# Performance work log

Hardware: AMD Instinct MI355X
Metric: run time of the kernel (lower is better)

Reference implementation:

```python
import jax, jax.numpy as jnp
import numpy as np

N, E, F, EB, NB, G = 50000, 800000, 64, 20, 3, 100
CUTOFF = 5.0
NUM_EMB = 119


def silu(x):
    return x * jax.nn.sigmoid(x)


def setup_inputs() -> dict:
    key = jax.random.key(0)
    ks = jax.random.split(key, 16)
    w = lambda k, shape, scale: jax.random.normal(k, shape, dtype=jnp.float32) * scale
    inp = {}
    # forward args
    inp["node_features"] = jax.random.randint(ks[0], (N,), 1, NUM_EMB)
    inp["node_positions"] = jax.random.normal(ks[1], (N, 3), dtype=jnp.float32)
    inp["edge_index"] = jax.random.randint(ks[2], (2, E), 0, N)
    inp["node_graph_index"] = jnp.sort(jax.random.randint(ks[3], (N,), 0, G))
    # learned parameters (stacked over NB interaction blocks)
    inp["emb"] = w(ks[4], (NUM_EMB, F), 1.0)
    inp["msg_W1"] = w(ks[5], (NB, F, F), F ** -0.5)
    inp["msg_b1"] = jnp.zeros((NB, F), jnp.float32)
    inp["msg_W2"] = w(ks[6], (NB, F, 3 * F), F ** -0.5)
    inp["msg_b2"] = jnp.zeros((NB, 3 * F), jnp.float32)
    inp["filt_W"] = w(ks[7], (NB, EB, 3 * F), EB ** -0.5)
    inp["filt_b"] = jnp.zeros((NB, 3 * F), jnp.float32)
    inp["upd_U"] = w(ks[8], (NB, F, F), F ** -0.5)
    inp["upd_V"] = w(ks[9], (NB, F, F), F ** -0.5)
    inp["upd_W1"] = w(ks[10], (NB, 2 * F, F), (2 * F) ** -0.5)
    inp["upd_b1"] = jnp.zeros((NB, F), jnp.float32)
    inp["upd_W2"] = w(ks[11], (NB, F, 3 * F), F ** -0.5)
    inp["upd_b2"] = jnp.zeros((NB, 3 * F), jnp.float32)
    # readout MLP: Linear(F,F) + SiLU + Linear(F,1)
    inp["ro_W1"] = w(ks[12], (F, F), F ** -0.5)
    inp["ro_b1"] = jnp.zeros((F,), jnp.float32)
    inp["ro_W2"] = w(ks[13], (F, 1), F ** -0.5)
    inp["ro_b2"] = jnp.zeros((1,), jnp.float32)
    return inp


def _painn_forward(node_positions, emb, msg_W1, msg_b1, msg_W2, msg_b2,
                   filt_W, filt_b, upd_U, upd_V, upd_W1, upd_b1, upd_W2, upd_b2,
                   ro_W1, ro_b1, ro_W2, ro_b2,
                   node_features, edge_index, node_graph_index):
    recv, send = edge_index[0], edge_index[1]  # row aggregates over col neighbors
    s = emb[node_features]                      # [N,F] scalar node states
    v = jnp.zeros((N, 3, F), s.dtype)           # [N,3,F] vector node states

    # edge geometry
    d = node_positions[send] - node_positions[recv]       # [E,3]
    r = jnp.sqrt(jnp.sum(d * d, axis=1, keepdims=True))   # [E,1]
    dhat = d / (r + 1e-10)                                # unit edge vectors

    # Bessel (sinc) radial basis expansion of edge norms: [E,EB]
    n = jnp.arange(1, EB + 1, dtype=s.dtype)
    rbf = jnp.sqrt(2.0 / CUTOFF) * jnp.sin(n * jnp.pi * r / CUTOFF) / (r + 1e-10)
    # smooth cosine cutoff: [E,1]
    fc = jnp.where(r < CUTOFF, 0.5 * (jnp.cos(jnp.pi * r / CUTOFF) + 1.0), 0.0)

    for b in range(NB):
        # --- message block ---
        phi = silu(s @ msg_W1[b] + msg_b1[b]) @ msg_W2[b] + msg_b2[b]   # [N,3F]
        Wf = (rbf @ filt_W[b] + filt_b[b]) * fc                          # [E,3F]
        m = phi[send] * Wf                                               # [E,3F]
        gate_v, gate_e, m_s = jnp.split(m, 3, axis=-1)                   # [E,F] each
        m_v = v[send] * gate_v[:, None, :] + dhat[:, :, None] * gate_e[:, None, :]  # [E,3,F]
        s = s + jax.ops.segment_sum(m_s, recv, num_segments=N)
        v = v + jax.ops.segment_sum(m_v, recv, num_segments=N)
        # --- update block ---
        Uv = jnp.einsum('ndf,fg->ndg', v, upd_U[b])                      # [N,3,F]
        Vv = jnp.einsum('ndf,fg->ndg', v, upd_V[b])                      # [N,3,F]
        Vn = jnp.sqrt(jnp.sum(Vv * Vv, axis=1) + 1e-8)                   # [N,F]
        a = silu(jnp.concatenate([s, Vn], axis=-1) @ upd_W1[b] + upd_b1[b]) @ upd_W2[b] + upd_b2[b]
        a_vv, a_sv, a_ss = jnp.split(a, 3, axis=-1)
        v = v + a_vv[:, None, :] * Uv
        s = s + a_sv * jnp.sum(Uv * Vv, axis=1) + a_ss

    # readout MLP + per-graph sum reduction
    ro = silu(s @ ro_W1 + ro_b1) @ ro_W2 + ro_b2                         # [N,1]
    graph_out = jax.ops.segment_sum(ro, node_graph_index, num_segments=G)  # [G,1]

    # graph Laplacian of final scalar states
    deg = jax.ops.segment_sum(jnp.ones((E,), s.dtype), recv, num_segments=N)  # [N]
    lap = deg[:, None] * s - jax.ops.segment_sum(s[send], recv, num_segments=N)  # [N,F]
    return graph_out, s, lap


def reference(node_features, node_positions, edge_index, node_graph_index,
              emb, msg_W1, msg_b1, msg_W2, msg_b2, filt_W, filt_b,
              upd_U, upd_V, upd_W1, upd_b1, upd_W2, upd_b2,
              ro_W1, ro_b1, ro_W2, ro_b2):
    return _painn_forward(node_positions, emb, msg_W1, msg_b1, msg_W2, msg_b2,
                          filt_W, filt_b, upd_U, upd_V, upd_W1, upd_b1, upd_W2, upd_b2,
                          ro_W1, ro_b1, ro_W2, ro_b2,
                          node_features, edge_index, node_graph_index)
```

## Files before the change

### kernel.cpp

```cpp
#include <hip/hip_runtime.h>

#define NN 50000
#define NE 800000
#define FF 64
#define EB 20
#define NBLK 3
#define NG 100

__device__ __forceinline__ float silu_f(float x) {
  return x / (1.f + expf(-x));
}

__global__ __launch_bounds__(256) void k_init(float4* v0, int* cnt, float* gout) {
  int i = blockIdx.x * blockDim.x + threadIdx.x;
  if (i < NN * 48) v0[i] = make_float4(0.f, 0.f, 0.f, 0.f);
  if (i < NN) cnt[i] = 0;
  if (i < NG) gout[i] = 0.f;
}

__global__ __launch_bounds__(256) void k_embed(const int* __restrict__ feat,
                                               const float* __restrict__ emb,
                                               const int* __restrict__ ei,
                                               float* __restrict__ s, int* cnt) {
  int i = blockIdx.x * blockDim.x + threadIdx.x;
  if (i < NN * FF) s[i] = emb[feat[i >> 6] * FF + (i & 63)];
  if (i < NE) atomicAdd(&cnt[ei[i]], 1);
}

__global__ __launch_bounds__(1024) void k_scan(const int* __restrict__ cnt,
                                               int* __restrict__ rowst,
                                               int* __restrict__ rowcur) {
  __shared__ int part[1024];
  int t = threadIdx.x;
  const int CH = 52;
  int base = t * CH;
  int own = 0;
  const int4* c4 = (const int4*)(cnt + base);
#pragma unroll
  for (int i = 0; i < CH / 4; i++) {
    int idx = base + i * 4;
    if (idx + 3 < NN) {
      int4 q = c4[i];
      own += q.x + q.y + q.z + q.w;
    } else {
      for (int j = 0; j < 4; j++)
        if (idx + j < NN) own += cnt[idx + j];
    }
  }
  part[t] = own;
  __syncthreads();
  for (int off = 1; off < 1024; off <<= 1) {
    int v = (t >= off) ? part[t - off] : 0;
    __syncthreads();
    part[t] += v;
    __syncthreads();
  }
  int excl = part[t] - own;
  for (int i = 0; i < CH; i++) {
    int idx = base + i;
    if (idx < NN) {
      rowst[idx] = excl;
      rowcur[idx] = excl;
      excl += cnt[idx];
    }
  }
  if (t == 1023) rowst[NN] = excl;
}

__global__ __launch_bounds__(256) void k_fillgeo(const int* __restrict__ ei,
                                                 const float* __restrict__ pos,
                                                 int* rowcur, float4* __restrict__ d4,
                                                 int* __restrict__ eid) {
  int e = blockIdx.x * blockDim.x + threadIdx.x;
  if (e >= NE) return;
  int rv = ei[e], sd = ei[NE + e];
  float dx = pos[sd * 3 + 0] - pos[rv * 3 + 0];
  float dy = pos[sd * 3 + 1] - pos[rv * 3 + 1];
  float dz = pos[sd * 3 + 2] - pos[rv * 3 + 2];
  float r = sqrtf(dx * dx + dy * dy + dz * dz);
  d4[e] = make_float4(dx, dy, dz, r);
  int slot = atomicAdd(&rowcur[rv], 1);
  eid[slot] = e;
}

__global__ __launch_bounds__(256) void k_rbf(const int* __restrict__ ei,
                                             const float4* __restrict__ d4,
                                             const int* __restrict__ eid,
                                             float4* __restrict__ geo,
                                             int* __restrict__ send_s,
                                             float* __restrict__ rbf2) {
  __shared__ float buf[256 * EB];
  int tid = threadIdx.x;
  int slot = blockIdx.x * 256 + tid;
  int e = eid[slot];
  float4 d = d4[e];
  float r = d.w;
  float inv = 1.f / (r + 1e-10f);
  float fc = (r < 5.0f) ? 0.5f * (cosf(0.6283185307179586f * r) + 1.f) : 0.f;
  geo[slot] = make_float4(d.x * inv, d.y * inv, d.z * inv, fc);
  send_s[slot] = ei[NE + e];
  float cs = 0.6324555320336759f * inv * fc;
#pragma unroll
  for (int k = 0; k < EB; k++)
    buf[tid * EB + k] = cs * sinf((float)(k + 1) * 0.6283185307179586f * r);
  __syncthreads();
  size_t base = (size_t)blockIdx.x * 256 * EB;
#pragma unroll
  for (int i = 0; i < EB; i++)
    rbf2[base + i * 256 + tid] = buf[i * 256 + tid];
}

__global__ __launch_bounds__(256) void k_phi1(const float* __restrict__ s,
                                              const float* __restrict__ W1,
                                              const float* __restrict__ b1,
                                              float* __restrict__ h) {
  int lane = threadIdx.x & 63;
  int gw = (blockIdx.x * blockDim.x + threadIdx.x) >> 6;
  int nw = (gridDim.x * blockDim.x) >> 6;
  float w[FF];
#pragma unroll
  for (int k = 0; k < FF; k++) w[k] = W1[k * FF + lane];
  float bb = b1[lane];
  for (int n0 = gw; n0 < NN; n0 += nw) {
    int n = __builtin_amdgcn_readfirstlane(n0);
    const float4* row = (const float4*)(s + (size_t)n * FF);
    float a0 = bb, a1 = 0.f, a2 = 0.f, a3 = 0.f;
#pragma unroll
    for (int q = 0; q < 16; q++) {
      float4 x = row[q];
      a0 = fmaf(x.x, w[4 * q], a0);
      a1 = fmaf(x.y, w[4 * q + 1], a1);
      a2 = fmaf(x.z, w[4 * q + 2], a2);
      a3 = fmaf(x.w, w[4 * q + 3], a3);
    }
    h[(size_t)n * FF + lane] = silu_f((a0 + a1) + (a2 + a3));
  }
}

__global__ __launch_bounds__(256) void k_phi2(const float* __restrict__ h,
                                              const float* __restrict__ W2,
                                              const float* __restrict__ b2,
                                              float3* __restrict__ phi3) {
  int lane = threadIdx.x & 63;
  int gw = (blockIdx.x * blockDim.x + threadIdx.x) >> 6;
  int nw = (gridDim.x * blockDim.x) >> 6;
  float w0[FF], w1[FF], w2[FF];
#pragma unroll
  for (int k = 0; k < FF; k++) {
    w0[k] = W2[k * 192 + lane];
    w1[k] = W2[k * 192 + 64 + lane];
    w2[k] = W2[k * 192 + 128 + lane];
  }
  float c0 = b2[lane], c1 = b2[64 + lane], c2 = b2[128 + lane];
  for (int n0 = gw; n0 < NN; n0 += nw) {
    int n = __builtin_amdgcn_readfirstlane(n0);
    const float4* row = (const float4*)(h + (size_t)n * FF);
    float a0 = c0, a1 = c1, a2 = c2;
#pragma unroll
    for (int q = 0; q < 16; q++) {
      float4 x = row[q];
      a0 = fmaf(x.x, w0[4 * q], a0);
      a1 = fmaf(x.x, w1[4 * q], a1);
      a2 = fmaf(x.x, w2[4 * q], a2);
      a0 = fmaf(x.y, w0[4 * q + 1], a0);
      a1 = fmaf(x.y, w1[4 * q + 1], a1);
      a2 = fmaf(x.y, w2[4 * q + 1], a2);
      a0 = fmaf(x.z, w0[4 * q + 2], a0);
      a1 = fmaf(x.z, w1[4 * q + 2], a1);
      a2 = fmaf(x.z, w2[4 * q + 2], a2);
      a0 = fmaf(x.w, w0[4 * q + 3], a0);
      a1 = fmaf(x.w, w1[4 * q + 3], a1);
      a2 = fmaf(x.w, w2[4 * q + 3], a2);
    }
    phi3[(size_t)n * FF + lane] = make_float3(a0, a1, a2);
  }
}

template <bool FIRST>
__global__ __launch_bounds__(256) void k_msg(const float3* __restrict__ phi3,
                                             const float3* __restrict__ v03,
                                             float* __restrict__ s,
                                             float3* __restrict__ v13,
                                             const float* __restrict__ fW,
                                             const float* __restrict__ fb,
                                             const float4* __restrict__ geo,
                                             const int* __restrict__ send_s,
                                             const int* __restrict__ rowst,
                                             const float* __restrict__ rbf2) {
  int lane = threadIdx.x & 63;
  int gw = (blockIdx.x * blockDim.x + threadIdx.x) >> 6;
  int nw = (gridDim.x * blockDim.x) >> 6;
  float fw0[EB], fw1[EB], fw2[EB];
#pragma unroll
  for (int k = 0; k < EB; k++) {
    if (!FIRST) fw0[k] = fW[k * 192 + lane];
    fw1[k] = fW[k * 192 + 64 + lane];
    fw2[k] = fW[k * 192 + 128 + lane];
  }
  float fb0 = fb[lane], fb1 = fb[64 + lane], fb2 = fb[128 + lane];
  for (int n0 = gw; n0 < NN; n0 += nw) {
    int n = __builtin_amdgcn_readfirstlane(n0);
    int beg = rowst[n], end = rowst[n + 1];
    float accs = 0.f, av0 = 0.f, av1 = 0.f, av2 = 0.f;
    for (int base = beg; base < end; base += 64) {
      int cnt = end - base;
      if (cnt > 64) cnt = 64;
      int jl = (base + lane < end) ? send_s[base + lane] : 0;
      int t = 0;
      for (; t + 2 <= cnt; t += 2) {
        int sA = base + t, sB = sA + 1;
        int jA = __builtin_amdgcn_readlane(jl, t);
        int jB = __builtin_amdgcn_readlane(jl, t + 1);
        float4 gA = geo[sA], gB = geo[sB];
        const float4* rA = (const float4*)(rbf2 + (size_t)sA * EB);
        const float4* rB = (const float4*)(rbf2 + (size_t)sB * EB);
        float4 qa0 = rA[0], qa1 = rA[1], qa2 = rA[2], qa3 = rA[3], qa4 = rA[4];
        float4 qb0 = rB[0], qb1 = rB[1], qb2 = rB[2], qb3 = rB[3], qb4 = rB[4];
        float3 pA = phi3[(size_t)jA * FF + lane];
        float3 pB = phi3[(size_t)jB * FF + lane];
        float3 vA, vB;
        if (!FIRST) {
          vA = v03[(size_t)jA * FF + lane];
          vB = v03[(size_t)jB * FF + lane];
        }
        float rbA[EB] = {qa0.x, qa0.y, qa0.z, qa0.w, qa1.x, qa1.y, qa1.z,
                         qa1.w, qa2.x, qa2.y, qa2.z, qa2.w, qa3.x, qa3.y,
                         qa3.z, qa3.w, qa4.x, qa4.y, qa4.z, qa4.w};
        float rbB[EB] = {qb0.x, qb0.y, qb0.z, qb0.w, qb1.x, qb1.y, qb1.z,
                         qb1.w, qb2.x, qb2.y, qb2.z, qb2.w, qb3.x, qb3.y,
                         qb3.z, qb3.w, qb4.x, qb4.y, qb4.z, qb4.w};
        float wf1A = fb1 * gA.w, wf2A = fb2 * gA.w;
#pragma unroll
        for (int k = 0; k < EB; k++) {
          wf1A = fmaf(rbA[k], fw1[k], wf1A);
          wf2A = fmaf(rbA[k], fw2[k], wf2A);
        }
        float geA = pA.y * wf1A;
        accs = fmaf(pA.z, wf2A, accs);
        if (!FIRST) {
          float wf0A = fb0 * gA.w;
#pragma unroll
          for (int k = 0; k < EB; k++) wf0A = fmaf(rbA[k], fw0[k], wf0A);
          float gvA = pA.x * wf0A;
          av0 = fmaf(vA.x, gvA, fmaf(gA.x, geA, av0));
          av1 = fmaf(vA.y, gvA, fmaf(gA.y, geA, av1));
          av2 = fmaf(vA.z, gvA, fmaf(gA.z, geA, av2));
        } else {
          av0 = fmaf(gA.x, geA, av0);
          av1 = fmaf(gA.y, geA, av1);
          av2 = fmaf(gA.z, geA, av2);
        }
        float wf1B = fb1 * gB.w, wf2B = fb2 * gB.w;
#pragma unroll
        for (int k = 0; k < EB; k++) {
          wf1B = fmaf(rbB[k], fw1[k], wf1B);
          wf2B = fmaf(rbB[k], fw2[k], wf2B);
        }
        float geB = pB.y * wf1B;
        accs = fmaf(pB.z, wf2B, accs);
        if (!FIRST) {
          float wf0B = fb0 * gB.w;
#pragma unroll
          for (int k = 0; k < EB; k++) wf0B = fmaf(rbB[k], fw0[k], wf0B);
          float gvB = pB.x * wf0B;
          av0 = fmaf(vB.x, gvB, fmaf(gB.x, geB, av0));
          av1 = fmaf(vB.y, gvB, fmaf(gB.y, geB, av1));
          av2 = fmaf(vB.z, gvB, fmaf(gB.z, geB, av2));
        } else {
          av0 = fmaf(gB.x, geB, av0);
          av1 = fmaf(gB.y, geB, av1);
          av2 = fmaf(gB.z, geB, av2);
        }
      }
      for (; t < cnt; t++) {
        int sA = base + t;
        int jA = __builtin_amdgcn_readlane(jl, t);
        float4 gA = geo[sA];
        const float4* rA = (const float4*)(rbf2 + (size_t)sA * EB);
        float4 qa0 = rA[0], qa1 = rA[1], qa2 = rA[2], qa3 = rA[3], qa4 = rA[4];
        float3 pA = phi3[(size_t)jA * FF + lane];
        float rbA[EB] = {qa0.x, qa0.y, qa0.z, qa0.w, qa1.x, qa1.y, qa1.z,
                         qa1.w, qa2.x, qa2.y, qa2.z, qa2.w, qa3.x, qa3.y,
                         qa3.z, qa3.w, qa4.x, qa4.y, qa4.z, qa4.w};
        float wf1A = fb1 * gA.w, wf2A = fb2 * gA.w;
#pragma unroll
        for (int k = 0; k < EB; k++) {
          wf1A = fmaf(rbA[k], fw1[k], wf1A);
          wf2A = fmaf(rbA[k], fw2[k], wf2A);
        }
        float geA = pA.y * wf1A;
        accs = fmaf(pA.z, wf2A, accs);
        if (!FIRST) {
          float wf0A = fb0 * gA.w;
#pragma unroll
          for (int k = 0; k < EB; k++) wf0A = fmaf(rbA[k], fw0[k], wf0A);
          float gvA = pA.x * wf0A;
          float3 vA = v03[(size_t)jA * FF + lane];
          av0 = fmaf(vA.x, gvA, fmaf(gA.x, geA, av0));
          av1 = fmaf(vA.y, gvA, fmaf(gA.y, geA, av1));
          av2 = fmaf(vA.z, gvA, fmaf(gA.z, geA, av2));
        } else {
          av0 = fmaf(gA.x, geA, av0);
          av1 = fmaf(gA.y, geA, av1);
          av2 = fmaf(gA.z, geA, av2);
        }
      }
    }
    s[(size_t)n * FF + lane] += accs;
    if (!FIRST) {
      float3 vo = v03[(size_t)n * FF + lane];
      v13[(size_t)n * FF + lane] =
          make_float3(vo.x + av0, vo.y + av1, vo.z + av2);
    } else {
      v13[(size_t)n * FF + lane] = make_float3(av0, av1, av2);
    }
  }
}

__global__ __launch_bounds__(256) void k_upd1(const float3* __restrict__ v13,
                                              const float* __restrict__ U,
                                              const float* __restrict__ V,
                                              float3* __restrict__ Uv3,
                                              float* __restrict__ Vn,
                                              float* __restrict__ dotUV) {
  int lane = threadIdx.x & 63;
  int gw = (blockIdx.x * blockDim.x + threadIdx.x) >> 6;
  int nw = (gridDim.x * blockDim.x) >> 6;
  float u[FF], w[FF];
#pragma unroll
  for (int k = 0; k < FF; k++) {
    u[k] = U[k * FF + lane];
    w[k] = V[k * FF + lane];
  }
  for (int n0 = gw; n0 < NN; n0 += nw) {
    int n = __builtin_amdgcn_readfirstlane(n0);
    const float4* row = (const float4*)((const float*)v13 + (size_t)n * 192);
    float uv0 = 0, uv1 = 0, uv2 = 0, vv0 = 0, vv1 = 0, vv2 = 0;
#pragma unroll
    for (int gq = 0; gq < 16; gq++) {
      float4 A = row[3 * gq], B = row[3 * gq + 1], C = row[3 * gq + 2];
      int k = 4 * gq;
      uv0 = fmaf(A.x, u[k], uv0); vv0 = fmaf(A.x, w[k], vv0);
      uv1 = fmaf(A.y, u[k], uv1); vv1 = fmaf(A.y, w[k], vv1);
      uv2 = fmaf(A.z, u[k], uv2); vv2 = fmaf(A.z, w[k], vv2);
      uv0 = fmaf(A.w, u[k + 1], uv0); vv0 = fmaf(A.w, w[k + 1], vv0);
      uv1 = fmaf(B.x, u[k + 1], uv1); vv1 = fmaf(B.x, w[k + 1], vv1);
      uv2 = fmaf(B.y, u[k + 1], uv2); vv2 = fmaf(B.y, w[k + 1], vv2);
      uv0 = fmaf(B.z, u[k + 2], uv0); vv0 = fmaf(B.z, w[k + 2], vv0);
      uv1 = fmaf(B.w, u[k + 2], uv1); vv1 = fmaf(B.w, w[k + 2], vv1);
      uv2 = fmaf(C.x, u[k + 2], uv2); vv2 = fmaf(C.x, w[k + 2], vv2);
      uv0 = fmaf(C.y, u[k + 3], uv0); vv0 = fmaf(C.y, w[k + 3], vv0);
      uv1 = fmaf(C.z, u[k + 3], uv1); vv1 = fmaf(C.z, w[k + 3], vv1);
      uv2 = fmaf(C.w, u[k + 3], uv2); vv2 = fmaf(C.w, w[k + 3], vv2);
    }
    Uv3[(size_t)n * FF + lane] = make_float3(uv0, uv1, uv2);
    Vn[(size_t)n * FF + lane] = sqrtf(vv0 * vv0 + vv1 * vv1 + vv2 * vv2 + 1e-8f);
    dotUV[(size_t)n * FF + lane] = uv0 * vv0 + uv1 * vv1 + uv2 * vv2;
  }
}

__global__ __launch_bounds__(256) void k_upd2(const float* __restrict__ s,
                                              const float* __restrict__ Vn,
                                              const float* __restrict__ W1,
                                              const float* __restrict__ b1,
                                              float* __restrict__ h) {
  int lane = threadIdx.x & 63;
  int gw = (blockIdx.x * blockDim.x + threadIdx.x) >> 6;
  int nw = (gridDim.x * blockDim.x) >> 6;
  float w[2 * FF];
#pragma unroll
  for (int k = 0; k < 2 * FF; k++) w[k] = W1[k * FF + lane];
  float bb = b1[lane];
  for (int n0 = gw; n0 < NN; n0 += nw) {
    int n = __builtin_amdgcn_readfirstlane(n0);
    const float4* rs = (const float4*)(s + (size_t)n * FF);
    const float4* rv = (const float4*)(Vn + (size_t)n * FF);
    float a0 = bb, a1 = 0.f, a2 = 0.f, a3 = 0.f;
#pragma unroll
    for (int q = 0; q < 16; q++) {
      float4 x = rs[q];
      a0 = fmaf(x.x, w[4 * q], a0);
      a1 = fmaf(x.y, w[4 * q + 1], a1);
      a2 = fmaf(x.z, w[4 * q + 2], a2);
      a3 = fmaf(x.w, w[4 * q + 3], a3);
    }
#pragma unroll
    for (int q = 0; q < 16; q++) {
      float4 x = rv[q];
      a0 = fmaf(x.x, w[FF + 4 * q], a0);
      a1 = fmaf(x.y, w[FF + 4 * q + 1], a1);
      a2 = fmaf(x.z, w[FF + 4 * q + 2], a2);
      a3 = fmaf(x.w, w[FF + 4 * q + 3], a3);
    }
    h[(size_t)n * FF + lane] = silu_f((a0 + a1) + (a2 + a3));
  }
}

__global__ __launch_bounds__(256) void k_upd3(const float* __restrict__ h,
                                              const float* __restrict__ W2,
                                              const float* __restrict__ b2,
                                              const float3* __restrict__ Uv3,
                                              const float3* __restrict__ v13,
                                              const float* __restrict__ dotUV,
                                              float3* __restrict__ v03,
                                              float* __restrict__ s) {
  int lane = threadIdx.x & 63;
  int gw = (blockIdx.x * blockDim.x + threadIdx.x) >> 6;
  int nw = (gridDim.x * blockDim.x) >> 6;
  float w0[FF], w1[FF], w2[FF];
#pragma unroll
  for (int k = 0; k < FF; k++) {
    w0[k] = W2[k * 192 + lane];
    w1[k] = W2[k * 192 + 64 + lane];
    w2[k] = W2[k * 192 + 128 + lane];
  }
  float c0 = b2[lane], c1 = b2[64 + lane], c2 = b2[128 + lane];
  for (int n0 = gw; n0 < NN; n0 += nw) {
    int n = __builtin_amdgcn_readfirstlane(n0);
    const float4* row = (const float4*)(h + (size_t)n * FF);
    float a0 = c0, a1 = c1, a2 = c2;
#pragma unroll
    for (int q = 0; q < 16; q++) {
      float4 x = row[q];
      a0 = fmaf(x.x, w0[4 * q], a0);
      a1 = fmaf(x.x, w1[4 * q], a1);
      a2 = fmaf(x.x, w2[4 * q], a2);
      a0 = fmaf(x.y, w0[4 * q + 1], a0);
      a1 = fmaf(x.y, w1[4 * q + 1], a1);
      a2 = fmaf(x.y, w2[4 * q + 1], a2);
      a0 = fmaf(x.z, w0[4 * q + 2], a0);
      a1 = fmaf(x.z, w1[4 * q + 2], a1);
      a2 = fmaf(x.z, w2[4 * q + 2], a2);
      a0 = fmaf(x.w, w0[4 * q + 3], a0);
      a1 = fmaf(x.w, w1[4 * q + 3], a1);
      a2 = fmaf(x.w, w2[4 * q + 3], a2);
    }
    float3 uv = Uv3[(size_t)n * FF + lane];
    float3 vv = v13[(size_t)n * FF + lane];
    v03[(size_t)n * FF + lane] = make_float3(
        fmaf(a0, uv.x, vv.x), fmaf(a0, uv.y, vv.y), fmaf(a0, uv.z, vv.z));
    size_t i_ = (size_t)n * FF + lane;
    s[i_] = fmaf(a1, dotUV[i_], s[i_] + a2);
  }
}

__global__ __launch_bounds__(256) void k_final(const float* __restrict__ s,
                                               const float* __restrict__ roW1,
                                               const float* __restrict__ rob1,
                                               const float* __restrict__ roW2,
                                               const float* __restrict__ rob2,
                                               const int* __restrict__ gidx,
                                               const int* __restrict__ rowst,
                                               const int* __restrict__ send_s,
                                               float* __restrict__ gout,
                                               float* __restrict__ lap) {
  int lane = threadIdx.x & 63;
  int gw = (blockIdx.x * blockDim.x + threadIdx.x) >> 6;
  int nw = (gridDim.x * blockDim.x) >> 6;
  float w[FF];
#pragma unroll
  for (int k = 0; k < FF; k++) w[k] = roW1[k * FF + lane];
  float b1v = rob1[lane], w2v = roW2[lane], b2v = rob2[0];
  for (int n0 = gw; n0 < NN; n0 += nw) {
    int n = __builtin_amdgcn_readfirstlane(n0);
    int beg = rowst[n], end = rowst[n + 1];
    float ac0 = 0.f, ac1 = 0.f, ac2 = 0.f, ac3 = 0.f;
    float ac4 = 0.f, ac5 = 0.f, ac6 = 0.f, ac7 = 0.f;
    for (int base = beg; base < end; base += 64) {
      int cnt = end - base;
      if (cnt > 64) cnt = 64;
      int jl = (base + lane < end) ? send_s[base + lane] : 0;
      int t = 0;
      for (; t + 8 <= cnt; t += 8) {
        int j0 = __builtin_amdgcn_readlane(jl, t);
        int j1 = __builtin_amdgcn_readlane(jl, t + 1);
        int j2 = __builtin_amdgcn_readlane(jl, t + 2);
        int j3 = __builtin_amdgcn_readlane(jl, t + 3);
        int j4 = __builtin_amdgcn_readlane(jl, t + 4);
        int j5 = __builtin_amdgcn_readlane(jl, t + 5);
        int j6 = __builtin_amdgcn_readlane(jl, t + 6);
        int j7 = __builtin_amdgcn_readlane(jl, t + 7);
        ac0 += s[(size_t)j0 * FF + lane];
        ac1 += s[(size_t)j1 * FF + lane];
        ac2 += s[(size_t)j2 * FF + lane];
        ac3 += s[(size_t)j3 * FF + lane];
        ac4 += s[(size_t)j4 * FF + lane];
        ac5 += s[(size_t)j5 * FF + lane];
        ac6 += s[(size_t)j6 * FF + lane];
        ac7 += s[(size_t)j7 * FF + lane];
      }
      for (; t < cnt; t++) {
        int j0 = __builtin_amdgcn_readlane(jl, t);
        ac0 += s[(size_t)j0 * FF + lane];
      }
    }
    float acc = ((ac0 + ac1) + (ac2 + ac3)) + ((ac4 + ac5) + (ac6 + ac7));
    float sv = s[(size_t)n * FF + lane];
    lap[(size_t)n * FF + lane] = (float)(end - beg) * sv - acc;
    const float4* row = (const float4*)(s + (size_t)n * FF);
    float a0 = b1v, a1 = 0.f, a2 = 0.f, a3 = 0.f;
#pragma unroll
    for (int q = 0; q < 16; q++) {
      float4 x = row[q];
      a0 = fmaf(x.x, w[4 * q], a0);
      a1 = fmaf(x.y, w[4 * q + 1], a1);
      a2 = fmaf(x.z, w[4 * q + 2], a2);
      a3 = fmaf(x.w, w[4 * q + 3], a3);
    }
    float c = silu_f((a0 + a1) + (a2 + a3)) * w2v;
#pragma unroll
    for (int off = 32; off > 0; off >>= 1) c += __shfl_down(c, off, 64);
    if (lane == 0) atomicAdd(&gout[gidx[n]], c + b2v);
  }
}

extern "C" void kernel_launch(void* const* d_in, const int* in_sizes, int n_in,
                              void* d_out, int out_size, void* d_ws, size_t ws_size,
                              hipStream_t stream) {
  const int* feat = (const int*)d_in[0];
  const float* pos = (const float*)d_in[1];
  const int* ei = (const int*)d_in[2];
  const int* gidx = (const int*)d_in[3];
  const float* emb = (const float*)d_in[4];
  const float* msgW1 = (const float*)d_in[5];
  const float* msgb1 = (const float*)d_in[6];
  const float* msgW2 = (const float*)d_in[7];
  const float* msgb2 = (const float*)d_in[8];
  const float* filtW = (const float*)d_in[9];
  const float* filtb = (const float*)d_in[10];
  const float* updU = (const float*)d_in[11];
  const float* updV = (const float*)d_in[12];
  const float* updW1 = (const float*)d_in[13];
  const float* updb1 = (const float*)d_in[14];
  const float* updW2 = (const float*)d_in[15];
  const float* updb2 = (const float*)d_in[16];
  const float* roW1 = (const float*)d_in[17];
  const float* rob1 = (const float*)d_in[18];
  const float* roW2 = (const float*)d_in[19];
  const float* rob2 = (const float*)d_in[20];

  float* gout = (float*)d_out;
  float* s = gout + NG;
  float* lap = s + (size_t)NN * FF;

  char* p = (char*)d_ws;
  auto alloc = [&](size_t bytes) {
    char* r = p;
    p += (bytes + 255) & ~(size_t)255;
    return r;
  };
  float3* v03 = (float3*)alloc((size_t)NN * 192 * 4);
  float3* v13 = (float3*)alloc((size_t)NN * 192 * 4);
  float3* phiUv3 = (float3*)alloc((size_t)NN * 192 * 4);
  float* h = (float*)alloc((size_t)NN * FF * 4);
  float* Vn = (float*)alloc((size_t)NN * FF * 4);
  float* dotUV = (float*)alloc((size_t)NN * FF * 4);
  float4* geo = (float4*)alloc((size_t)NE * 16);
  float4* d4 = (float4*)alloc((size_t)NE * 16);
  float* rbf2 = (float*)alloc((size_t)NE * EB * 4);
  int* send_s = (int*)alloc((size_t)NE * 4);
  int* eid = (int*)alloc((size_t)NE * 4);
  int* rowst = (int*)alloc((size_t)(NN + 1) * 4);
  int* rowcur = (int*)alloc((size_t)NN * 4);
  int* cnt = (int*)alloc((size_t)NN * 4);

  k_init<<<(NN * 48 + 255) / 256, 256, 0, stream>>>((float4*)v03, cnt, gout);
  k_embed<<<(NN * FF + 255) / 256, 256, 0, stream>>>(feat, emb, ei, s, cnt);
  k_scan<<<1, 1024, 0, stream>>>(cnt, rowst, rowcur);
  k_fillgeo<<<NE / 256, 256, 0, stream>>>(ei, pos, rowcur, d4, eid);
  k_rbf<<<NE / 256, 256, 0, stream>>>(ei, d4, eid, geo, send_s, rbf2);

  for (int b = 0; b < NBLK; b++) {
    k_phi1<<<1024, 256, 0, stream>>>(s, msgW1 + b * FF * FF, msgb1 + b * FF, h);
    k_phi2<<<1024, 256, 0, stream>>>(h, msgW2 + b * FF * 192, msgb2 + b * 192,
                                     phiUv3);
    if (b == 0)
      k_msg<true><<<4096, 256, 0, stream>>>(phiUv3, v03, s, v13,
                                            filtW + b * EB * 192,
                                            filtb + b * 192, geo, send_s,
                                            rowst, rbf2);
    else
      k_msg<false><<<4096, 256, 0, stream>>>(phiUv3, v03, s, v13,
                                             filtW + b * EB * 192,
                                             filtb + b * 192, geo, send_s,
                                             rowst, rbf2);
    k_upd1<<<1024, 256, 0, stream>>>(v13, updU + b * FF * FF, updV + b * FF * FF,
                                     phiUv3, Vn, dotUV);
    k_upd2<<<1024, 256, 0, stream>>>(s, Vn, updW1 + b * 2 * FF * FF,
                                     updb1 + b * FF, h);
    k_upd3<<<1024, 256, 0, stream>>>(h, updW2 + b * FF * 192, updb2 + b * 192,
                                     phiUv3, v13, dotUV, v03, s);
  }

  k_final<<<4096, 256, 0, stream>>>(s, roW1, rob1, roW2, rob2, gidx, rowst,
                                    send_s, gout, lap);
}
```

Baseline: 2.008 ms.

## Broadcast row elements via readlane instead of redundant per-lane row loads

Result: slower. 2.071 ms (+3.2%).

```diff
diff --git a/kernel.cpp b/kernel.cpp
--- a/kernel.cpp
+++ b/kernel.cpp
@@ -7,6 +7,9 @@
 #define NBLK 3
 #define NG 100
 
+__device__ __forceinline__ float bcastf(float v, int k) {
+  return __int_as_float(__builtin_amdgcn_readlane(__float_as_int(v), k));
+}
 __device__ __forceinline__ float silu_f(float x) {
   return x / (1.f + expf(-x));
 }
@@ -123,15 +126,14 @@
   float bb = b1[lane];
   for (int n0 = gw; n0 < NN; n0 += nw) {
     int n = __builtin_amdgcn_readfirstlane(n0);
-    const float4* row = (const float4*)(s + (size_t)n * FF);
+    float sv = s[(size_t)n * FF + lane];
     float a0 = bb, a1 = 0.f, a2 = 0.f, a3 = 0.f;
 #pragma unroll
-    for (int q = 0; q < 16; q++) {
-      float4 x = row[q];
-      a0 = fmaf(x.x, w[4 * q], a0);
-      a1 = fmaf(x.y, w[4 * q + 1], a1);
-      a2 = fmaf(x.z, w[4 * q + 2], a2);
-      a3 = fmaf(x.w, w[4 * q + 3], a3);
+    for (int k = 0; k < FF; k += 4) {
+      a0 = fmaf(bcastf(sv, k), w[k], a0);
+      a1 = fmaf(bcastf(sv, k + 1), w[k + 1], a1);
+      a2 = fmaf(bcastf(sv, k + 2), w[k + 2], a2);
+      a3 = fmaf(bcastf(sv, k + 3), w[k + 3], a3);
     }
     h[(size_t)n * FF + lane] = silu_f((a0 + a1) + (a2 + a3));
   }
@@ -154,23 +156,14 @@
   float c0 = b2[lane], c1 = b2[64 + lane], c2 = b2[128 + lane];
   for (int n0 = gw; n0 < NN; n0 += nw) {
     int n = __builtin_amdgcn_readfirstlane(n0);
-    const float4* row = (const float4*)(h + (size_t)n * FF);
+    float hv = h[(size_t)n * FF + lane];
     float a0 = c0, a1 = c1, a2 = c2;
 #pragma unroll
-    for (int q = 0; q < 16; q++) {
-      float4 x = row[q];
-      a0 = fmaf(x.x, w0[4 * q], a0);
-      a1 = fmaf(x.x, w1[4 * q], a1);
-      a2 = fmaf(x.x, w2[4 * q], a2);
-      a0 = fmaf(x.y, w0[4 * q + 1], a0);
-      a1 = fmaf(x.y, w1[4 * q + 1], a1);
-      a2 = fmaf(x.y, w2[4 * q + 1], a2);
-      a0 = fmaf(x.z, w0[4 * q + 2], a0);
-      a1 = fmaf(x.z, w1[4 * q + 2], a1);
-      a2 = fmaf(x.z, w2[4 * q + 2], a2);
-      a0 = fmaf(x.w, w0[4 * q + 3], a0);
-      a1 = fmaf(x.w, w1[4 * q + 3], a1);
-      a2 = fmaf(x.w, w2[4 * q + 3], a2);
+    for (int k = 0; k < FF; k++) {
+      float hk = bcastf(hv, k);
+      a0 = fmaf(hk, w0[k], a0);
+      a1 = fmaf(hk, w1[k], a1);
+      a2 = fmaf(hk, w2[k], a2);
     }
     phi3[(size_t)n * FF + lane] = make_float3(a0, a1, a2);
   }
@@ -212,10 +205,8 @@
         int jA = __builtin_amdgcn_readlane(jl, t);
         int jB = __builtin_amdgcn_readlane(jl, t + 1);
         float4 gA = geo[sA], gB = geo[sB];
-        const float4* rA = (const float4*)(rbf2 + (size_t)sA * EB);
-        const float4* rB = (const float4*)(rbf2 + (size_t)sB * EB);
-        float4 qa0 = rA[0], qa1 = rA[1], qa2 = rA[2], qa3 = rA[3], qa4 = rA[4];
-        float4 qb0 = rB[0], qb1 = rB[1], qb2 = rB[2], qb3 = rB[3], qb4 = rB[4];
+        float rA = (lane < EB) ? rbf2[(size_t)sA * EB + lane] : 0.f;
+        float rB = (lane < EB) ? rbf2[(size_t)sB * EB + lane] : 0.f;
         float3 pA = phi3[(size_t)jA * FF + lane];
         float3 pB = phi3[(size_t)jB * FF + lane];
         float3 vA, vB;
@@ -223,24 +214,17 @@
           vA = v03[(size_t)jA * FF + lane];
           vB = v03[(size_t)jB * FF + lane];
         }
-        float rbA[EB] = {qa0.x, qa0.y, qa0.z, qa0.w, qa1.x, qa1.y, qa1.z,
-                         qa1.w, qa2.x, qa2.y, qa2.z, qa2.w, qa3.x, qa3.y,
-                         qa3.z, qa3.w, qa4.x, qa4.y, qa4.z, qa4.w};
-        float rbB[EB] = {qb0.x, qb0.y, qb0.z, qb0.w, qb1.x, qb1.y, qb1.z,
-                         qb1.w, qb2.x, qb2.y, qb2.z, qb2.w, qb3.x, qb3.y,
-                         qb3.z, qb3.w, qb4.x, qb4.y, qb4.z, qb4.w};
-        float wf1A = fb1 * gA.w, wf2A = fb2 * gA.w;
+        float wf0A = fb0 * gA.w, wf1A = fb1 * gA.w, wf2A = fb2 * gA.w;
 #pragma unroll
         for (int k = 0; k < EB; k++) {
-          wf1A = fmaf(rbA[k], fw1[k], wf1A);
-          wf2A = fmaf(rbA[k], fw2[k], wf2A);
+          float rk = bcastf(rA, k);
+          if (!FIRST) wf0A = fmaf(rk, fw0[k], wf0A);
+          wf1A = fmaf(rk, fw1[k], wf1A);
+          wf2A = fmaf(rk, fw2[k], wf2A);
         }
         float geA = pA.y * wf1A;
         accs = fmaf(pA.z, wf2A, accs);
         if (!FIRST) {
-          float wf0A = fb0 * gA.w;
-#pragma unroll
-          for (int k = 0; k < EB; k++) wf0A = fmaf(rbA[k], fw0[k], wf0A);
           float gvA = pA.x * wf0A;
           av0 = fmaf(vA.x, gvA, fmaf(gA.x, geA, av0));
           av1 = fmaf(vA.y, gvA, fmaf(gA.y, geA, av1));
@@ -250,18 +234,17 @@
           av1 = fmaf(gA.y, geA, av1);
           av2 = fmaf(gA.z, geA, av2);
         }
-        float wf1B = fb1 * gB.w, wf2B = fb2 * gB.w;
+        float wf0B = fb0 * gB.w, wf1B = fb1 * gB.w, wf2B = fb2 * gB.w;
 #pragma unroll
         for (int k = 0; k < EB; k++) {
-          wf1B = fmaf(rbB[k], fw1[k], wf1B);
-          wf2B = fmaf(rbB[k], fw2[k], wf2B);
+          float rk = bcastf(rB, k);
+          if (!FIRST) wf0B = fmaf(rk, fw0[k], wf0B);
+          wf1B = fmaf(rk, fw1[k], wf1B);
+          wf2B = fmaf(rk, fw2[k], wf2B);
         }
         float geB = pB.y * wf1B;
         accs = fmaf(pB.z, wf2B, accs);
         if (!FIRST) {
-          float wf0B = fb0 * gB.w;
-#pragma unroll
-          for (int k = 0; k < EB; k++) wf0B = fmaf(rbB[k], fw0[k], wf0B);
           float gvB = pB.x * wf0B;
           av0 = fmaf(vB.x, gvB, fmaf(gB.x, geB, av0));
           av1 = fmaf(vB.y, gvB, fmaf(gB.y, geB, av1));
@@ -276,24 +259,19 @@
         int sA = base + t;
         int jA = __builtin_amdgcn_readlane(jl, t);
         float4 gA = geo[sA];
-        const float4* rA = (const float4*)(rbf2 + (size_t)sA * EB);
-        float4 qa0 = rA[0], qa1 = rA[1], qa2 = rA[2], qa3 = rA[3], qa4 = rA[4];
+        float rA = (lane < EB) ? rbf2[(size_t)sA * EB + lane] : 0.f;
         float3 pA = phi3[(size_t)jA * FF + lane];
-        float rbA[EB] = {qa0.x, qa0.y, qa0.z, qa0.w, qa1.x, qa1.y, qa1.z,
-                         qa1.w, qa2.x, qa2.y, qa2.z, qa2.w, qa3.x, qa3.y,
-                         qa3.z, qa3.w, qa4.x, qa4.y, qa4.z, qa4.w};
-        float wf1A = fb1 * gA.w, wf2A = fb2 * gA.w;
+        float wf0A = fb0 * gA.w, wf1A = fb1 * gA.w, wf2A = fb2 * gA.w;
 #pragma unroll
         for (int k = 0; k < EB; k++) {
-          wf1A = fmaf(rbA[k], fw1[k], wf1A);
-          wf2A = fmaf(rbA[k], fw2[k], wf2A);
+          float rk = bcastf(rA, k);
+          if (!FIRST) wf0A = fmaf(rk, fw0[k], wf0A);
+          wf1A = fmaf(rk, fw1[k], wf1A);
+          wf2A = fmaf(rk, fw2[k], wf2A);
         }
         float geA = pA.y * wf1A;
         accs = fmaf(pA.z, wf2A, accs);
         if (!FIRST) {
-          float wf0A = fb0 * gA.w;
-#pragma unroll
-          for (int k = 0; k < EB; k++) wf0A = fmaf(rbA[k], fw0[k], wf0A);
           float gvA = pA.x * wf0A;
           float3 vA = v03[(size_t)jA * FF + lane];
           av0 = fmaf(vA.x, gvA, fmaf(gA.x, geA, av0));
@@ -334,24 +312,13 @@
   }
   for (int n0 = gw; n0 < NN; n0 += nw) {
     int n = __builtin_amdgcn_readfirstlane(n0);
-    const float4* row = (const float4*)((const float*)v13 + (size_t)n * 192);
+    float3 xv = v13[(size_t)n * FF + lane];
     float uv0 = 0, uv1 = 0, uv2 = 0, vv0 = 0, vv1 = 0, vv2 = 0;
 #pragma unroll
-    for (int gq = 0; gq < 16; gq++) {
-      float4 A = row[3 * gq], B = row[3 * gq + 1], C = row[3 * gq + 2];
-      int k = 4 * gq;
-      uv0 = fmaf(A.x, u[k], uv0); vv0 = fmaf(A.x, w[k], vv0);
-      uv1 = fmaf(A.y, u[k], uv1); vv1 = fmaf(A.y, w[k], vv1);
-      uv2 = fmaf(A.z, u[k], uv2); vv2 = fmaf(A.z, w[k], vv2);
-      uv0 = fmaf(A.w, u[k + 1], uv0); vv0 = fmaf(A.w, w[k + 1], vv0);
-      uv1 = fmaf(B.x, u[k + 1], uv1); vv1 = fmaf(B.x, w[k + 1], vv1);
-      uv2 = fmaf(B.y, u[k + 1], uv2); vv2 = fmaf(B.y, w[k + 1], vv2);
-      uv0 = fmaf(B.z, u[k + 2], uv0); vv0 = fmaf(B.z, w[k + 2], vv0);
-      uv1 = fmaf(B.w, u[k + 2], uv1); vv1 = fmaf(B.w, w[k + 2], vv1);
-      uv2 = fmaf(C.x, u[k + 2], uv2); vv2 = fmaf(C.x, w[k + 2], vv2);
-      uv0 = fmaf(C.y, u[k + 3], uv0); vv0 = fmaf(C.y, w[k + 3], vv0);
-      uv1 = fmaf(C.z, u[k + 3], uv1); vv1 = fmaf(C.z, w[k + 3], vv1);
-      uv2 = fmaf(C.w, u[k + 3], uv2); vv2 = fmaf(C.w, w[k + 3], vv2);
+    for (int k = 0; k < FF; k++) {
+      float a0 = bcastf(xv.x, k), a1 = bcastf(xv.y, k), a2 = bcastf(xv.z, k);
+      uv0 = fmaf(a0, u[k], uv0); uv1 = fmaf(a1, u[k], uv1); uv2 = fmaf(a2, u[k], uv2);
+      vv0 = fmaf(a0, w[k], vv0); vv1 = fmaf(a1, w[k], vv1); vv2 = fmaf(a2, w[k], vv2);
     }
     Uv3[(size_t)n * FF + lane] = make_float3(uv0, uv1, uv2);
     Vn[(size_t)n * FF + lane] = sqrtf(vv0 * vv0 + vv1 * vv1 + vv2 * vv2 + 1e-8f);
@@ -373,24 +340,22 @@
   float bb = b1[lane];
   for (int n0 = gw; n0 < NN; n0 += nw) {
     int n = __builtin_amdgcn_readfirstlane(n0);
-    const float4* rs = (const float4*)(s + (size_t)n * FF);
-    const float4* rv = (const float4*)(Vn + (size_t)n * FF);
+    float sv = s[(size_t)n * FF + lane];
+    float vn = Vn[(size_t)n * FF + lane];
     float a0 = bb, a1 = 0.f, a2 = 0.f, a3 = 0.f;
 #pragma unroll
-    for (int q = 0; q < 16; q++) {
-      float4 x = rs[q];
-      a0 = fmaf(x.x, w[4 * q], a0);
-      a1 = fmaf(x.y, w[4 * q + 1], a1);
-      a2 = fmaf(x.z, w[4 * q + 2], a2);
-      a3 = fmaf(x.w, w[4 * q + 3], a3);
-    }
-#pragma unroll
-    for (int q = 0; q < 16; q++) {
-      float4 x = rv[q];
-      a0 = fmaf(x.x, w[FF + 4 * q], a0);
-      a1 = fmaf(x.y, w[FF + 4 * q + 1], a1);
-      a2 = fmaf(x.z, w[FF + 4 * q + 2], a2);
-      a3 = fmaf(x.w, w[FF + 4 * q + 3], a3);
+    for (int k = 0; k < FF; k += 4) {
+      a0 = fmaf(bcastf(sv, k), w[k], a0);
+      a1 = fmaf(bcastf(sv, k + 1), w[k + 1], a1);
+      a2 = fmaf(bcastf(sv, k + 2), w[k + 2], a2);
+      a3 = fmaf(bcastf(sv, k + 3), w[k + 3], a3);
+    }
+#pragma unroll
+    for (int k = 0; k < FF; k += 4) {
+      a0 = fmaf(bcastf(vn, k), w[FF + k], a0);
+      a1 = fmaf(bcastf(vn, k + 1), w[FF + k + 1], a1);
+      a2 = fmaf(bcastf(vn, k + 2), w[FF + k + 2], a2);
+      a3 = fmaf(bcastf(vn, k + 3), w[FF + k + 3], a3);
     }
     h[(size_t)n * FF + lane] = silu_f((a0 + a1) + (a2 + a3));
   }
@@ -417,23 +382,14 @@
   float c0 = b2[lane], c1 = b2[64 + lane], c2 = b2[128 + lane];
   for (int n0 = gw; n0 < NN; n0 += nw) {
     int n = __builtin_amdgcn_readfirstlane(n0);
-    const float4* row = (const float4*)(h + (size_t)n * FF);
+    float hv = h[(size_t)n * FF + lane];
     float a0 = c0, a1 = c1, a2 = c2;
 #pragma unroll
-    for (int q = 0; q < 16; q++) {
-      float4 x = row[q];
-      a0 = fmaf(x.x, w0[4 * q], a0);
-      a1 = fmaf(x.x, w1[4 * q], a1);
-      a2 = fmaf(x.x, w2[4 * q], a2);
-      a0 = fmaf(x.y, w0[4 * q + 1], a0);
-      a1 = fmaf(x.y, w1[4 * q + 1], a1);
-      a2 = fmaf(x.y, w2[4 * q + 1], a2);
-      a0 = fmaf(x.z, w0[4 * q + 2], a0);
-      a1 = fmaf(x.z, w1[4 * q + 2], a1);
-      a2 = fmaf(x.z, w2[4 * q + 2], a2);
-      a0 = fmaf(x.w, w0[4 * q + 3], a0);
-      a1 = fmaf(x.w, w1[4 * q + 3], a1);
-      a2 = fmaf(x.w, w2[4 * q + 3], a2);
+    for (int k = 0; k < FF; k++) {
+      float hk = bcastf(hv, k);
+      a0 = fmaf(hk, w0[k], a0);
+      a1 = fmaf(hk, w1[k], a1);
+      a2 = fmaf(hk, w2[k], a2);
     }
     float3 uv = Uv3[(size_t)n * FF + lane];
     float3 vv = v13[(size_t)n * FF + lane];
@@ -455,6 +411,8 @@
                                                float* __restrict__ gout,
                                                float* __restrict__ lap) {
   int lane = threadIdx.x & 63;
+  int grp = lane >> 4;
+  int fl = lane & 15;
   int gw = (blockIdx.x * blockDim.x + threadIdx.x) >> 6;
   int nw = (gridDim.x * blockDim.x) >> 6;
   float w[FF];
@@ -464,48 +422,40 @@
   for (int n0 = gw; n0 < NN; n0 += nw) {
     int n = __builtin_amdgcn_readfirstlane(n0);
     int beg = rowst[n], end = rowst[n + 1];
-    float ac0 = 0.f, ac1 = 0.f, ac2 = 0.f, ac3 = 0.f;
-    float ac4 = 0.f, ac5 = 0.f, ac6 = 0.f, ac7 = 0.f;
-    for (int base = beg; base < end; base += 64) {
-      int cnt = end - base;
-      if (cnt > 64) cnt = 64;
-      int jl = (base + lane < end) ? send_s[base + lane] : 0;
-      int t = 0;
-      for (; t + 8 <= cnt; t += 8) {
-        int j0 = __builtin_amdgcn_readlane(jl, t);
-        int j1 = __builtin_amdgcn_readlane(jl, t + 1);
-        int j2 = __builtin_amdgcn_readlane(jl, t + 2);
-        int j3 = __builtin_amdgcn_readlane(jl, t + 3);
-        int j4 = __builtin_amdgcn_readlane(jl, t + 4);
-        int j5 = __builtin_amdgcn_readlane(jl, t + 5);
-        int j6 = __builtin_amdgcn_readlane(jl, t + 6);
-        int j7 = __builtin_amdgcn_readlane(jl, t + 7);
-        ac0 += s[(size_t)j0 * FF + lane];
-        ac1 += s[(size_t)j1 * FF + lane];
-        ac2 += s[(size_t)j2 * FF + lane];
-        ac3 += s[(size_t)j3 * FF + lane];
-        ac4 += s[(size_t)j4 * FF + lane];
-        ac5 += s[(size_t)j5 * FF + lane];
-        ac6 += s[(size_t)j6 * FF + lane];
-        ac7 += s[(size_t)j7 * FF + lane];
-      }
-      for (; t < cnt; t++) {
-        int j0 = __builtin_amdgcn_readlane(jl, t);
-        ac0 += s[(size_t)j0 * FF + lane];
-      }
-    }
-    float acc = ((ac0 + ac1) + (ac2 + ac3)) + ((ac4 + ac5) + (ac6 + ac7));
+    int deg = end - beg;
+    float ax = 0.f, ay = 0.f, az = 0.f, aw = 0.f;
+    int tE = (deg + 3) >> 2;
+    for (int t = 0; t < tE; t++) {
+      int si = beg + (t << 2) + grp;
+      int ok = si < end;
+      int j = ok ? send_s[si] : 0;
+      float m = ok ? 1.f : 0.f;
+      const float4* rp = (const float4*)(s + (size_t)j * FF);
+      float4 xv = rp[fl];
+      ax = fmaf(m, xv.x, ax);
+      ay = fmaf(m, xv.y, ay);
+      az = fmaf(m, xv.z, az);
+      aw = fmaf(m, xv.w, aw);
+    }
+    ax += __shfl_xor(ax, 16, 64); ax += __shfl_xor(ax, 32, 64);
+    ay += __shfl_xor(ay, 16, 64); ay += __shfl_xor(ay, 32, 64);
+    az += __shfl_xor(az, 16, 64); az += __shfl_xor(az, 32, 64);
+    aw += __shfl_xor(aw, 16, 64); aw += __shfl_xor(aw, 32, 64);
+    float degf = (float)deg;
+    if (lane < 16) {
+      float4 sv4 = ((const float4*)(s + (size_t)n * FF))[fl];
+      float4 o = make_float4(fmaf(degf, sv4.x, -ax), fmaf(degf, sv4.y, -ay),
+                             fmaf(degf, sv4.z, -az), fmaf(degf, sv4.w, -aw));
+      ((float4*)(lap + (size_t)n * FF))[fl] = o;
+    }
     float sv = s[(size_t)n * FF + lane];
-    lap[(size_t)n * FF + lane] = (float)(end - beg) * sv - acc;
-    const float4* row = (const float4*)(s + (size_t)n * FF);
     float a0 = b1v, a1 = 0.f, a2 = 0.f, a3 = 0.f;
 #pragma unroll
-    for (int q = 0; q < 16; q++) {
-      float4 x = row[q];
-      a0 = fmaf(x.x, w[4 * q], a0);
-      a1 = fmaf(x.y, w[4 * q + 1], a1);
-      a2 = fmaf(x.z, w[4 * q + 2], a2);
-      a3 = fmaf(x.w, w[4 * q + 3], a3);
+    for (int k = 0; k < FF; k += 4) {
+      a0 = fmaf(bcastf(sv, k), w[k], a0);
+      a1 = fmaf(bcastf(sv, k + 1), w[k + 1], a1);
+      a2 = fmaf(bcastf(sv, k + 2), w[k + 2], a2);
+      a3 = fmaf(bcastf(sv, k + 3), w[k + 3], a3);
     }
     float c = silu_f((a0 + a1) + (a2 + a3)) * w2v;
 #pragma unroll
@@ -571,8 +521,8 @@
   k_rbf<<<NE / 256, 256, 0, stream>>>(ei, d4, eid, geo, send_s, rbf2);
 
   for (int b = 0; b < NBLK; b++) {
-    k_phi1<<<1024, 256, 0, stream>>>(s, msgW1 + b * FF * FF, msgb1 + b * FF, h);
-    k_phi2<<<1024, 256, 0, stream>>>(h, msgW2 + b * FF * 192, msgb2 + b * 192,
+    k_phi1<<<2048, 256, 0, stream>>>(s, msgW1 + b * FF * FF, msgb1 + b * FF, h);
+    k_phi2<<<2048, 256, 0, stream>>>(h, msgW2 + b * FF * 192, msgb2 + b * 192,
                                      phiUv3);
     if (b == 0)
       k_msg<true><<<4096, 256, 0, stream>>>(phiUv3, v03, s, v13,
@@ -584,11 +534,11 @@
                                              filtW + b * EB * 192,
                                              filtb + b * 192, geo, send_s,
                                              rowst, rbf2);
-    k_upd1<<<1024, 256, 0, stream>>>(v13, updU + b * FF * FF, updV + b * FF * FF,
+    k_upd1<<<2048, 256, 0, stream>>>(v13, updU + b * FF * FF, updV + b * FF * FF,
                                      phiUv3, Vn, dotUV);
-    k_upd2<<<1024, 256, 0, stream>>>(s, Vn, updW1 + b * 2 * FF * FF,
+    k_upd2<<<2048, 256, 0, stream>>>(s, Vn, updW1 + b * 2 * FF * FF,
                                      updb1 + b * FF, h);
-    k_upd3<<<1024, 256, 0, stream>>>(h, updW2 + b * FF * 192, updb2 + b * 192,
+    k_upd3<<<2048, 256, 0, stream>>>(h, updW2 + b * FF * 192, updb2 + b * 192,
                                      phiUv3, v13, dotUV, v03, s);
   }
 
```
